# Kernel tuning notes

Hardware: AMD Instinct MI355X
Metric: run time of the kernel (lower is better)

The kernel has to match this reference:

```python
import jax, jax.numpy as jnp
import numpy as np
import math

B, S, D = 2, 4096, 1024
H, HD = 16, 64
R = 16

def _rope(x, cos, sin):
    # x: [B, S, H, HD]; cos/sin: [S, HD//2]
    xr = x.reshape(*x.shape[:-1], HD // 2, 2)
    xe, xo = xr[..., 0], xr[..., 1]
    c = cos[None, :, None, :]
    s = sin[None, :, None, :]
    # complex multiply (xe + i*xo) * (c + i*s)
    re = xe * c - xo * s
    im = xe * s + xo * c
    return jnp.stack([re, im], axis=-1).reshape(x.shape)

def setup_inputs() -> dict:
    key = jax.random.key(0)
    ks = jax.random.split(key, 20)
    inp = {}
    inp["x"] = jax.random.normal(ks[0], (B, S, D), dtype=jnp.float32)
    pos = jnp.arange(S, dtype=jnp.float32)
    inv_freq = 1.0 / (10000.0 ** (jnp.arange(0, HD, 2, dtype=jnp.float32) / HD))
    ang = pos[:, None] * inv_freq[None, :]  # [S, HD//2]
    inp["freqs_cos"] = jnp.cos(ang)
    inp["freqs_sin"] = jnp.sin(ang)
    causal = jnp.triu(jnp.full((S, S), -1e9, dtype=jnp.float32), k=1)
    inp["mask"] = causal[None, None, :, :]
    sc = 1.0 / math.sqrt(D)
    inp["wq_w"] = jax.random.normal(ks[1], (D, D), dtype=jnp.float32) * sc
    inp["wq_b"] = jnp.zeros((D,), dtype=jnp.float32)
    inp["wk_w"] = jax.random.normal(ks[2], (D, D), dtype=jnp.float32) * sc
    inp["wv_w"] = jax.random.normal(ks[3], (D, D), dtype=jnp.float32) * sc
    inp["wo_w"] = jax.random.normal(ks[4], (D, D), dtype=jnp.float32) * sc
    inp["wo_b"] = jnp.zeros((D,), dtype=jnp.float32)
    for i, nm in enumerate(["q", "k", "v", "o"]):
        inp[f"lora_{nm}_l1"] = jax.random.normal(ks[5 + 2 * i], (R, D), dtype=jnp.float32) * sc
        inp[f"lora_{nm}_l2"] = jax.random.normal(ks[6 + 2 * i], (D, R), dtype=jnp.float32) * 0.01
    return inp

def reference(x, freqs_cos, freqs_sin, mask, wq_w, wq_b, wk_w, wv_w, wo_w, wo_b,
              lora_q_l1, lora_q_l2, lora_k_l1, lora_k_l2,
              lora_v_l1, lora_v_l2, lora_o_l1, lora_o_l2):
    # QKV projections + LoRA deltas (torch Linear: y = x @ W.T + b, W is [out, in])
    xq = x @ wq_w.T + wq_b + (x @ lora_q_l1.T) @ lora_q_l2.T
    xk = x @ wk_w.T + (x @ lora_k_l1.T) @ lora_k_l2.T
    xv = x @ wv_w.T + (x @ lora_v_l1.T) @ lora_v_l2.T
    xq = xq.reshape(B, S, H, HD)
    xk = xk.reshape(B, S, H, HD)
    xv = xv.reshape(B, S, H, HD)
    xq = _rope(xq, freqs_cos, freqs_sin)
    xk = _rope(xk, freqs_cos, freqs_sin)
    # attention (training path: keys/values = current xk/xv, causal mask additive)
    scores = jnp.einsum('bqhd,bkhd->bhqk', xq, xk) / math.sqrt(HD)
    scores = scores + mask
    probs = jax.nn.softmax(scores.astype(jnp.float32), axis=-1).astype(xq.dtype)
    out = jnp.einsum('bhqk,bkhd->bqhd', probs, xv).reshape(B, S, D)
    return out @ wo_w.T + wo_b + (out @ lora_o_l1.T) @ lora_o_l2.T
```

## Files before the change

kernel.cpp:

```cpp
#include <hip/hip_runtime.h>
#include <hip/hip_bf16.h>
#include <stdint.h>

#define S_DIM 4096
#define D_DIM 1024
#define M_ROWS 8192

typedef short bf16x8 __attribute__((ext_vector_type(8)));
typedef float f32x4  __attribute__((ext_vector_type(4)));

__device__ __forceinline__ f32x4 mfma16(bf16x8 a, bf16x8 b, f32x4 c) {
  return __builtin_amdgcn_mfma_f32_16x16x32_bf16(a, b, c, 0, 0, 0);
}
__device__ __forceinline__ short f2bs(float f) {
  __hip_bfloat16 h = __float2bfloat16(f);
  return *reinterpret_cast<short*>(&h);
}
__device__ __forceinline__ short f2bs_fast(float f) {
  unsigned u = __builtin_bit_cast(unsigned, f) + 0x8000u;
  return (short)(u >> 16);
}
__device__ __forceinline__ unsigned pk2bf(float a, float b) {
  unsigned ua = __builtin_bit_cast(unsigned, a) + 0x8000u;
  unsigned ub = __builtin_bit_cast(unsigned, b) + 0x8000u;
  return __builtin_amdgcn_perm(ub, ua, 0x07060302);
}
__device__ __forceinline__ float fexp2(float x) {
  return __builtin_amdgcn_exp2f(x);
}
__device__ __forceinline__ void gload16(const void* g, void* l) {
  __builtin_amdgcn_global_load_lds(
      (const __attribute__((address_space(1))) unsigned int*)g,
      (__attribute__((address_space(3))) unsigned int*)l, 16, 0, 0);
}

__global__ void prep_k(const float* __restrict__ x,
                       const float* __restrict__ wq, const float* __restrict__ wk,
                       const float* __restrict__ wv, const float* __restrict__ wo,
                       const float* __restrict__ wqb,
                       const float* __restrict__ lq1, const float* __restrict__ lq2,
                       const float* __restrict__ lk1, const float* __restrict__ lk2,
                       const float* __restrict__ lv1, const float* __restrict__ lv2,
                       const float* __restrict__ lo1, const float* __restrict__ lo2,
                       const float* __restrict__ cf, const float* __restrict__ sf,
                       short* __restrict__ xaug, short* __restrict__ wqkv,
                       short* __restrict__ woeff,
                       float* __restrict__ biasc, float* __restrict__ cs2)
{
  unsigned i = blockIdx.x * 256u + threadIdx.x;
  if (i < 8388608u) {
    xaug[i] = f2bs(x[i]);
    return;
  }
  i -= 8388608u;
  if (i < 3145728u) {
    unsigned n = i >> 10, k = i & 1023u;
    const float *wsrc, *l1, *l2;
    unsigned nn;
    if (n < 1024u)      { wsrc = wq; l1 = lq1; l2 = lq2; nn = n; }
    else if (n < 2048u) { wsrc = wk; l1 = lk1; l2 = lk2; nn = n - 1024u; }
    else                { wsrc = wv; l1 = lv1; l2 = lv2; nn = n - 2048u; }
    float v = wsrc[nn * 1024u + k];
#pragma unroll
    for (unsigned r = 0; r < 16u; ++r)
      v += l2[nn * 16u + r] * l1[r * 1024u + k];
    wqkv[i] = f2bs(v);
    return;
  }
  i -= 3145728u;
  if (i < 1048576u) {
    unsigned n = i >> 10, k = i & 1023u;
    float v = wo[i];
#pragma unroll
    for (unsigned r = 0; r < 16u; ++r)
      v += lo2[n * 16u + r] * lo1[r * 1024u + k];
    woeff[i] = f2bs(v);
    return;
  }
  i -= 1048576u;
  if (i < 3072u) {
    biasc[i] = (i < 1024u) ? wqb[i] : 0.f;
    return;
  }
  i -= 3072u;
  if (i < 131072u) {
    cs2[2u * i]     = cf[i];
    cs2[2u * i + 1] = sf[i];
  }
}

template<int MODE>
__global__ __launch_bounds__(256) void gemm_bt(
    const short* __restrict__ A, int lda,
    const short* __restrict__ B, int ldb,
    int N, int K,
    const float* __restrict__ bias,
    void* __restrict__ Cout, int ldc, int colofs,
    short* __restrict__ qo, short* __restrict__ ko, short* __restrict__ vo,
    const float* __restrict__ cs2)
{
  __shared__ short As[2][128 * 64];
  __shared__ short Bs[2][128 * 64];
  const int tid = threadIdx.x;
  const int w = tid >> 6, lane = tid & 63;
  const int q4 = lane >> 4, c = lane & 15;
  const int mh = w >> 1, nh = w & 1;

  const int id = (int)blockIdx.y * gridDim.x + (int)blockIdx.x;
  const int g = id & 7, j = id >> 3;
  const int mt = g * 8 + (j & 7);
  const int nt = j >> 3;

  const int l8 = lane >> 3, l7 = lane & 7;
  const int sw = (l7 ^ l8) * 8;
  const int c7 = c & 7;
  const short* Ags[4];
  const short* Bgs[4];
#pragma unroll
  for (int t = 0; t < 4; ++t) {
    Ags[t] = A + (size_t)(mt * 128 + (w * 4 + t) * 8 + l8) * lda + sw;
    Bgs[t] = B + (size_t)(nt * 128 + (w * 4 + t) * 8 + l8) * ldb + sw;
  }
  const int sDb = (w * 4) * 512;

  f32x4 acc[4][4];
#pragma unroll
  for (int ms = 0; ms < 4; ++ms)
#pragma unroll
    for (int ns = 0; ns < 4; ++ns) acc[ms][ns] = (f32x4){0.f, 0.f, 0.f, 0.f};

#pragma unroll
  for (int t = 0; t < 4; ++t) {
    gload16(Ags[t], &As[0][sDb + t * 512]);
    gload16(Bgs[t], &Bs[0][sDb + t * 512]);
    Ags[t] += 64; Bgs[t] += 64;
  }
  __syncthreads();

  const int nkt = K >> 6;
  for (int kt = 0; kt < nkt; ++kt) {
    const int cur = kt & 1, nxt = cur ^ 1;
    if (kt + 1 < nkt) {
#pragma unroll
      for (int t = 0; t < 4; ++t) {
        gload16(Ags[t], &As[nxt][sDb + t * 512]);
        gload16(Bgs[t], &Bs[nxt][sDb + t * 512]);
        Ags[t] += 64; Bgs[t] += 64;
      }
    }
#pragma unroll
    for (int s = 0; s < 2; ++s) {
      const int ch = ((s * 4 + q4) ^ c7) * 8;
      bf16x8 af[4], bfr[4];
#pragma unroll
      for (int ms = 0; ms < 4; ++ms)
        af[ms] = *(const bf16x8*)&As[cur][(mh * 64 + ms * 16 + c) * 64 + ch];
#pragma unroll
      for (int ns = 0; ns < 4; ++ns)
        bfr[ns] = *(const bf16x8*)&Bs[cur][(nh * 64 + ns * 16 + c) * 64 + ch];
#pragma unroll
      for (int ms = 0; ms < 4; ++ms)
#pragma unroll
        for (int ns = 0; ns < 4; ++ns)
          acc[ms][ns] = mfma16(af[ms], bfr[ns], acc[ms][ns]);
    }
    __syncthreads();
  }

#pragma unroll
  for (int ms = 0; ms < 4; ++ms) {
#pragma unroll
    for (int ns = 0; ns < 4; ++ns) {
      const int n = nt * 128 + nh * 64 + ns * 16 + c;
      if (MODE == 0) {
        float bsv = (n < N) ? bias[n] : 0.f;
        float* Co = (float*)Cout;
#pragma unroll
        for (int r = 0; r < 4; ++r) {
          int m = mt * 128 + mh * 64 + ms * 16 + q4 * 4 + r;
          if (n < N) Co[(size_t)m * ldc + n] = acc[ms][ns][r] + bsv;
        }
      } else if (MODE == 1) {
        short* Co = (short*)Cout;
#pragma unroll
        for (int r = 0; r < 4; ++r) {
          int m = mt * 128 + mh * 64 + ms * 16 + q4 * 4 + r;
          if (n < N) Co[(size_t)m * ldc + colofs + n] = f2bs_fast(acc[ms][ns][r]);
        }
      } else {
        float bsv = bias[n];
        int which = n >> 10;
        int m0 = mt * 128 + mh * 64 + ms * 16 + q4 * 4;
        int bb = m0 >> 12, spos = m0 & 4095;
        if (which < 2) {
          int h = (n >> 6) & 15;
          int hd = n & 63;
          short* dst = which == 0 ? qo : ko;
          const float sgn = (c & 1) ? 1.f : -1.f;
          const int ihalf = hd >> 1;
#pragma unroll
          for (int r = 0; r < 4; ++r) {
            float val = acc[ms][ns][r] + bsv;
            float part = __shfl_xor(val, 1);
            float2 cs = *(const float2*)&cs2[((size_t)(spos + r) * 32 + ihalf) * 2];
            float res = val * cs.x + part * (sgn * cs.y);
            if (which == 0) res *= 0.18033688011112042f;
            dst[(size_t)((bb * 16 + h) * 4096 + spos + r) * 64 + hd] = f2bs_fast(res);
          }
        } else {
          int h = (n >> 6) & 15;
          int hd = n & 63;
          uint2 vk;
          vk.x = pk2bf(acc[ms][ns][0] + bsv, acc[ms][ns][1] + bsv);
          vk.y = pk2bf(acc[ms][ns][2] + bsv, acc[ms][ns][3] + bsv);
          *(uint2*)&vo[(((size_t)bb * 16 + h) * 64 + hd) * 4096 + spos] = vk;
        }
      }
    }
  }
}

__global__ __launch_bounds__(256, 2) void flash_k(
    const short* __restrict__ Qb, const short* __restrict__ Kb,
    const short* __restrict__ Vt, short* __restrict__ Oaug)
{
  __shared__ short lds[24576];
  short* const PL = &lds[16384];

  const int id = (int)blockIdx.y * 16 + (int)blockIdx.x;
  const int g = id & 7, j = id >> 3;
  const int bh = g * 4 + (j >> 4);
  const int bx = j & 15;

  const int tid = threadIdx.x;
  const int w = tid >> 6, lane = tid & 63;
  const int q4 = lane >> 4, c = lane & 15;

  const short* Kg = Kb + (size_t)bh * 4096 * 64;
  const short* Vg = Vt + (size_t)bh * 64 * 4096;

  const int l8 = lane >> 3, l7 = lane & 7;
  const int sw = (l7 ^ l8) * 8;
  const int G0 = w * 2, G1 = w * 2 + 1;
  const int koff0 = (G0 * 8 + l8) * 64 + sw;
  const int koff1 = (G1 * 8 + l8) * 64 + sw;
  const int voff0 = (G0 * 8 + l8) * 4096 + sw;
  const int voff1 = (G1 * 8 + l8) * 4096 + sw;
  const int qg = w * 4;
  const int qoff0 = ((qg + 0) * 8 + l8) * 64 + sw;
  const int qoff1 = ((qg + 1) * 8 + l8) * 64 + sw;
  const int qoff2 = ((qg + 2) * 8 + l8) * 64 + sw;
  const int qoff3 = ((qg + 3) * 8 + l8) * 64 + sw;

  const int c7 = c & 7;
  const int chA0 = ((q4) ^ c7) * 8;
  const int chA1 = ((4 + q4) ^ c7) * 8;
  const int rowc = c * 64;
  const int rowq = (w * 16 + c) * 64;
  const int pw_base = (w * 16 + c) * 64 + (q4 & 1) * 4;
  const int pw_g = q4 >> 1;

  const int b = bh >> 4, h = bh & 15;

  for (int half = 0; half < 2; ++half) {
    const int qt = half == 0 ? 31 - bx : bx;
    const short* Qg = Qb + ((size_t)bh * 4096 + qt * 128) * 64;

    gload16(Qg + qoff0, &lds[16384 + (qg + 0) * 512]);
    gload16(Qg + qoff1, &lds[16384 + (qg + 1) * 512]);
    gload16(Qg + qoff2, &lds[16384 + (qg + 2) * 512]);
    gload16(Qg + qoff3, &lds[16384 + (qg + 3) * 512]);
    gload16(Kg + koff0, &lds[G0 * 512]);
    gload16(Kg + koff1, &lds[G1 * 512]);
    gload16(Vg + voff0, &lds[8192 + G0 * 512]);
    gload16(Vg + voff1, &lds[8192 + G1 * 512]);
    __syncthreads();

    bf16x8 qa0 = *(const bf16x8*)(PL + rowq + chA0);
    bf16x8 qa1 = *(const bf16x8*)(PL + rowq + chA1);
    bf16x8 qb0 = *(const bf16x8*)(PL + 4096 + rowq + chA0);
    bf16x8 qb1 = *(const bf16x8*)(PL + 4096 + rowq + chA1);

    f32x4 oa[4], ob[4];
#pragma unroll
    for (int i = 0; i < 4; ++i) {
      oa[i] = (f32x4){0.f, 0.f, 0.f, 0.f};
      ob[i] = (f32x4){0.f, 0.f, 0.f, 0.f};
    }
    float la = 0.f, lb = 0.f;

    const int last = 2 * qt + 1;
    for (int kt = 0; kt <= last; ++kt) {
      const int cur = (kt & 1) * 4096;
      const short* Kc = &lds[cur];
      const short* Vc = &lds[8192 + cur];
      if (kt < last) {
        const int nxt = ((kt + 1) & 1) * 4096;
        const short* ks = Kg + (size_t)(kt + 1) * 4096;
        const short* vs = Vg + (size_t)(kt + 1) * 64;
        gload16(ks + koff0, &lds[nxt + G0 * 512]);
        gload16(ks + koff1, &lds[nxt + G1 * 512]);
        gload16(vs + voff0, &lds[8192 + nxt + G0 * 512]);
        gload16(vs + voff1, &lds[8192 + nxt + G1 * 512]);
      }
      const bool doA = (kt <= 2 * qt);

      f32x4 sa[4], sb[4];
#pragma unroll
      for (int ns = 0; ns < 4; ++ns) {
        bf16x8 kf0 = *(const bf16x8*)(Kc + ns * 1024 + rowc + chA0);
        bf16x8 kf1 = *(const bf16x8*)(Kc + ns * 1024 + rowc + chA1);
        sa[ns] = mfma16(kf0, qa0, (f32x4){0.f, 0.f, 0.f, 0.f});
        sa[ns] = mfma16(kf1, qa1, sa[ns]);
        sb[ns] = mfma16(kf0, qb0, (f32x4){0.f, 0.f, 0.f, 0.f});
        sb[ns] = mfma16(kf1, qb1, sb[ns]);
      }
      if (kt == 2 * qt) {
#pragma unroll
        for (int ns = 0; ns < 4; ++ns)
#pragma unroll
          for (int r = 0; r < 4; ++r)
            if (ns * 16 + q4 * 4 + r > w * 16 + c) sa[ns][r] = -1e30f;
      }
      if (kt == last) {
#pragma unroll
        for (int ns = 0; ns < 4; ++ns)
#pragma unroll
          for (int r = 0; r < 4; ++r)
            if (ns * 16 + q4 * 4 + r > w * 16 + c) sb[ns][r] = -1e30f;
      }

      bf16x8 pfa0, pfa1;
      if (doA) {
        float ps[4][4];
#pragma unroll
        for (int ns = 0; ns < 4; ++ns)
#pragma unroll
          for (int r = 0; r < 4; ++r) ps[ns][r] = fexp2(sa[ns][r]);
        float s0 = (ps[0][0] + ps[0][1]) + (ps[0][2] + ps[0][3]);
        float s1 = (ps[1][0] + ps[1][1]) + (ps[1][2] + ps[1][3]);
        float s2 = (ps[2][0] + ps[2][1]) + (ps[2][2] + ps[2][3]);
        float s3 = (ps[3][0] + ps[3][1]) + (ps[3][2] + ps[3][3]);
        float sum = (s0 + s1) + (s2 + s3);
        sum += __shfl_xor(sum, 16);
        sum += __shfl_xor(sum, 32);
        la += sum;
#pragma unroll
        for (int ns = 0; ns < 4; ++ns) {
          uint2 pk;
          pk.x = pk2bf(ps[ns][0], ps[ns][1]);
          pk.y = pk2bf(ps[ns][2], ps[ns][3]);
          *(uint2*)(PL + pw_base + (((ns * 2 + pw_g) ^ c7) * 8)) = pk;
        }
        pfa0 = *(const bf16x8*)(PL + rowq + chA0);
        pfa1 = *(const bf16x8*)(PL + rowq + chA1);
      }
      {
        float ps[4][4];
#pragma unroll
        for (int ns = 0; ns < 4; ++ns)
#pragma unroll
          for (int r = 0; r < 4; ++r) ps[ns][r] = fexp2(sb[ns][r]);
        float s0 = (ps[0][0] + ps[0][1]) + (ps[0][2] + ps[0][3]);
        float s1 = (ps[1][0] + ps[1][1]) + (ps[1][2] + ps[1][3]);
        float s2 = (ps[2][0] + ps[2][1]) + (ps[2][2] + ps[2][3]);
        float s3 = (ps[3][0] + ps[3][1]) + (ps[3][2] + ps[3][3]);
        float sum = (s0 + s1) + (s2 + s3);
        sum += __shfl_xor(sum, 16);
        sum += __shfl_xor(sum, 32);
        lb += sum;
#pragma unroll
        for (int ns = 0; ns < 4; ++ns) {
          uint2 pk;
          pk.x = pk2bf(ps[ns][0], ps[ns][1]);
          pk.y = pk2bf(ps[ns][2], ps[ns][3]);
          *(uint2*)(PL + 4096 + pw_base + (((ns * 2 + pw_g) ^ c7) * 8)) = pk;
        }
      }
      bf16x8 pfb0 = *(const bf16x8*)(PL + 4096 + rowq + chA0);
      bf16x8 pfb1 = *(const bf16x8*)(PL + 4096 + rowq + chA1);

#pragma unroll
      for (int nc = 0; nc < 4; ++nc) {
        bf16x8 vf0 = *(const bf16x8*)(Vc + nc * 1024 + rowc + chA0);
        bf16x8 vf1 = *(const bf16x8*)(Vc + nc * 1024 + rowc + chA1);
        if (doA) {
          oa[nc] = mfma16(vf0, pfa0, oa[nc]);
          oa[nc] = mfma16(vf1, pfa1, oa[nc]);
        }
        ob[nc] = mfma16(vf0, pfb0, ob[nc]);
        ob[nc] = mfma16(vf1, pfb1, ob[nc]);
      }
      __syncthreads();
    }

    float lia = 1.f / la, lib = 1.f / lb;
#pragma unroll
    for (int nc = 0; nc < 4; ++nc) {
      uint2 ok;
      ok.x = pk2bf(oa[nc][0] * lia, oa[nc][1] * lia);
      ok.y = pk2bf(oa[nc][2] * lia, oa[nc][3] * lia);
      *(uint2*)(PL + pw_base + (((nc * 2 + pw_g) ^ c7) * 8)) = ok;
      uint2 ok2;
      ok2.x = pk2bf(ob[nc][0] * lib, ob[nc][1] * lib);
      ok2.y = pk2bf(ob[nc][2] * lib, ob[nc][3] * lib);
      *(uint2*)(PL + 4096 + pw_base + (((nc * 2 + pw_g) ^ c7) * 8)) = ok2;
    }
    __syncthreads();
#pragma unroll
    for (int i2 = 0; i2 < 4; ++i2) {
      int ch = tid + i2 * 256;
      int r = ch >> 3, g2 = ch & 7;
      size_t row = (size_t)b * 4096 + qt * 128 + r;
      *(int4*)&Oaug[row * 1024 + h * 64 + g2 * 8] =
          *(const int4*)(PL + r * 64 + ((g2 ^ (r & 7)) * 8));
    }
    __syncthreads();
  }
}

extern "C" void kernel_launch(void* const* d_in, const int* in_sizes, int n_in,
                              void* d_out, int out_size, void* d_ws, size_t ws_size,
                              hipStream_t stream) {
  const float* x   = (const float*)d_in[0];
  const float* fc  = (const float*)d_in[1];
  const float* fs  = (const float*)d_in[2];
  const float* wq  = (const float*)d_in[4];
  const float* wqb = (const float*)d_in[5];
  const float* wk  = (const float*)d_in[6];
  const float* wv  = (const float*)d_in[7];
  const float* wo  = (const float*)d_in[8];
  const float* wob = (const float*)d_in[9];
  const float* lq1 = (const float*)d_in[10];
  const float* lq2 = (const float*)d_in[11];
  const float* lk1 = (const float*)d_in[12];
  const float* lk2 = (const float*)d_in[13];
  const float* lv1 = (const float*)d_in[14];
  const float* lv2 = (const float*)d_in[15];
  const float* lo1 = (const float*)d_in[16];
  const float* lo2 = (const float*)d_in[17];

  char* ws = (char*)d_ws;
  const size_t OFF_XAUG  = 0;
  const size_t OFF_XOAUG = 16777216;
  const size_t OFF_WQKV  = 33554432;
  const size_t OFF_WOEFF = 39845888;
  const size_t OFF_BIASC = 41943040;
  const size_t OFF_QB    = 41955328;
  const size_t OFF_KB    = 58732544;
  const size_t OFF_VT    = 75509760;
  const size_t OFF_CS    = 92286976;

  short* xaug  = (short*)(ws + OFF_XAUG);
  short* xoaug = (short*)(ws + OFF_XOAUG);
  short* wqkv  = (short*)(ws + OFF_WQKV);
  short* woeff = (short*)(ws + OFF_WOEFF);
  float* biasc = (float*)(ws + OFF_BIASC);
  short* qb    = (short*)(ws + OFF_QB);
  short* kb    = (short*)(ws + OFF_KB);
  short* vt    = (short*)(ws + OFF_VT);
  float* cs2   = (float*)(ws + OFF_CS);

  prep_k<<<49676, 256, 0, stream>>>(x, wq, wk, wv, wo, wqb,
                                    lq1, lq2, lk1, lk2, lv1, lv2, lo1, lo2,
                                    fc, fs,
                                    xaug, wqkv, woeff, biasc, cs2);
  gemm_bt<2><<<dim3(24, 64), 256, 0, stream>>>(xaug, 1024, wqkv, 1024, 3072, 1024,
                                               biasc, nullptr, 0, 0, qb, kb, vt,
                                               cs2);
  flash_k<<<dim3(16, 32), 256, 0, stream>>>(qb, kb, vt, xoaug);
  gemm_bt<0><<<dim3(8, 64), 256, 0, stream>>>(xoaug, 1024, woeff, 1024, 1024, 1024,
                                              wob, d_out, 1024, 0,
                                              nullptr, nullptr, nullptr, nullptr);
}
```

Baseline: 367.1 us.

## Feed softmax probabilities directly from registers into PV MFMA via 16x16x16 layout

Computes P·V with the 16x16x16 bf16 MFMA, using the probability accumulator layout directly as the A operand. This removes the LDS round trip (store then reload) for the P tiles in every key iteration. The price is twice as many MFMA instructions, each with half the K depth, and transposed output fragments. Those fragments need per-row normalisation through shuffles and scalar 2-byte LDS stores in the epilogue.

```diff
diff --git a/kernel.cpp b/kernel.cpp
--- a/kernel.cpp
+++ b/kernel.cpp
@@ -7,10 +7,14 @@
 #define M_ROWS 8192
 
 typedef short bf16x8 __attribute__((ext_vector_type(8)));
+typedef short bf16x4 __attribute__((ext_vector_type(4)));
 typedef float f32x4  __attribute__((ext_vector_type(4)));
 
 __device__ __forceinline__ f32x4 mfma16(bf16x8 a, bf16x8 b, f32x4 c) {
   return __builtin_amdgcn_mfma_f32_16x16x32_bf16(a, b, c, 0, 0, 0);
+}
+__device__ __forceinline__ f32x4 mfma16x16(bf16x4 a, bf16x4 b, f32x4 c) {
+  return __builtin_amdgcn_mfma_f32_16x16x16bf16_1k(a, b, c, 0, 0, 0);
 }
 __device__ __forceinline__ short f2bs(float f) {
   __hip_bfloat16 h = __float2bfloat16(f);
@@ -24,6 +28,11 @@
   unsigned ua = __builtin_bit_cast(unsigned, a) + 0x8000u;
   unsigned ub = __builtin_bit_cast(unsigned, b) + 0x8000u;
   return __builtin_amdgcn_perm(ub, ua, 0x07060302);
+}
+__device__ __forceinline__ bf16x4 pk4(float a, float b, float c, float d) {
+  unsigned lo = pk2bf(a, b), hi = pk2bf(c, d);
+  unsigned long long both = ((unsigned long long)hi << 32) | (unsigned long long)lo;
+  return __builtin_bit_cast(bf16x4, both);
 }
 __device__ __forceinline__ float fexp2(float x) {
   return __builtin_amdgcn_exp2f(x);
@@ -257,8 +266,11 @@
   const int chA1 = ((4 + q4) ^ c7) * 8;
   const int rowc = c * 64;
   const int rowq = (w * 16 + c) * 64;
-  const int pw_base = (w * 16 + c) * 64 + (q4 & 1) * 4;
-  const int pw_g = q4 >> 1;
+  const int q4h = q4 >> 1, q4l = q4 & 1;
+  int vcol[4];
+#pragma unroll
+  for (int ns = 0; ns < 4; ++ns)
+    vcol[ns] = (((2 * ns + q4h) ^ c7) * 8) + q4l * 4;
 
   const int b = bh >> 4, h = bh & 15;
 
@@ -330,7 +342,7 @@
             if (ns * 16 + q4 * 4 + r > w * 16 + c) sb[ns][r] = -1e30f;
       }
 
-      bf16x8 pfa0, pfa1;
+      bf16x4 paf[4], pbf[4];
       if (doA) {
         float ps[4][4];
 #pragma unroll
@@ -346,14 +358,8 @@
         sum += __shfl_xor(sum, 32);
         la += sum;
 #pragma unroll
-        for (int ns = 0; ns < 4; ++ns) {
-          uint2 pk;
-          pk.x = pk2bf(ps[ns][0], ps[ns][1]);
-          pk.y = pk2bf(ps[ns][2], ps[ns][3]);
-          *(uint2*)(PL + pw_base + (((ns * 2 + pw_g) ^ c7) * 8)) = pk;
-        }
-        pfa0 = *(const bf16x8*)(PL + rowq + chA0);
-        pfa1 = *(const bf16x8*)(PL + rowq + chA1);
+        for (int ns = 0; ns < 4; ++ns)
+          paf[ns] = pk4(ps[ns][0], ps[ns][1], ps[ns][2], ps[ns][3]);
       }
       {
         float ps[4][4];
@@ -370,41 +376,38 @@
         sum += __shfl_xor(sum, 32);
         lb += sum;
 #pragma unroll
+        for (int ns = 0; ns < 4; ++ns)
+          pbf[ns] = pk4(ps[ns][0], ps[ns][1], ps[ns][2], ps[ns][3]);
+      }
+
+#pragma unroll
+      for (int nc = 0; nc < 4; ++nc) {
+        const short* vb = Vc + nc * 1024 + rowc;
+#pragma unroll
         for (int ns = 0; ns < 4; ++ns) {
-          uint2 pk;
-          pk.x = pk2bf(ps[ns][0], ps[ns][1]);
-          pk.y = pk2bf(ps[ns][2], ps[ns][3]);
-          *(uint2*)(PL + 4096 + pw_base + (((ns * 2 + pw_g) ^ c7) * 8)) = pk;
+          bf16x4 vf = *(const bf16x4*)(vb + vcol[ns]);
+          if (doA) oa[nc] = mfma16x16(paf[ns], vf, oa[nc]);
+          ob[nc] = mfma16x16(pbf[ns], vf, ob[nc]);
         }
       }
-      bf16x8 pfb0 = *(const bf16x8*)(PL + 4096 + rowq + chA0);
-      bf16x8 pfb1 = *(const bf16x8*)(PL + 4096 + rowq + chA1);
-
-#pragma unroll
-      for (int nc = 0; nc < 4; ++nc) {
-        bf16x8 vf0 = *(const bf16x8*)(Vc + nc * 1024 + rowc + chA0);
-        bf16x8 vf1 = *(const bf16x8*)(Vc + nc * 1024 + rowc + chA1);
-        if (doA) {
-          oa[nc] = mfma16(vf0, pfa0, oa[nc]);
-          oa[nc] = mfma16(vf1, pfa1, oa[nc]);
-        }
-        ob[nc] = mfma16(vf0, pfb0, ob[nc]);
-        ob[nc] = mfma16(vf1, pfb1, ob[nc]);
-      }
       __syncthreads();
     }
 
-    float lia = 1.f / la, lib = 1.f / lb;
+    float lar[4], lbr[4];
+#pragma unroll
+    for (int r = 0; r < 4; ++r) {
+      lar[r] = 1.f / __shfl(la, q4 * 4 + r);
+      lbr[r] = 1.f / __shfl(lb, q4 * 4 + r);
+    }
 #pragma unroll
     for (int nc = 0; nc < 4; ++nc) {
-      uint2 ok;
-      ok.x = pk2bf(oa[nc][0] * lia, oa[nc][1] * lia);
-      ok.y = pk2bf(oa[nc][2] * lia, oa[nc][3] * lia);
-      *(uint2*)(PL + pw_base + (((nc * 2 + pw_g) ^ c7) * 8)) = ok;
-      uint2 ok2;
-      ok2.x = pk2bf(ob[nc][0] * lib, ob[nc][1] * lib);
-      ok2.y = pk2bf(ob[nc][2] * lib, ob[nc][3] * lib);
-      *(uint2*)(PL + 4096 + pw_base + (((nc * 2 + pw_g) ^ c7) * 8)) = ok2;
+#pragma unroll
+      for (int r = 0; r < 4; ++r) {
+        const int row = w * 16 + q4 * 4 + r;
+        const int col = (((2 * nc + (c >> 3)) ^ (row & 7)) * 8) + (c & 7);
+        PL[row * 64 + col]        = f2bs_fast(oa[nc][r] * lar[r]);
+        PL[4096 + row * 64 + col] = f2bs_fast(ob[nc][r] * lbr[r]);
+      }
     }
     __syncthreads();
 #pragma unroll
```

New measurement: 371.1 us. Within noise of the previous version (+1.1%).
